# Kernel optimization log

Hardware: AMD Instinct MI355X
Metric: run time of the kernel (lower is better)

Reference implementation:

```python
import jax, jax.numpy as jnp
import numpy as np

B, T, N, D = 256, 200, 8, 64
MODEL = N * D          # 512
FFN_H = 1024 * N // 4  # 2048
EPS = 1.1920929e-07    # torch.finfo(float32).eps (nn.RMSNorm default eps=None)


def setup_inputs() -> dict:
    key = jax.random.key(0)
    ks = jax.random.split(key, 9)
    def xavier(k, shape):
        fan_in, fan_out = shape[-2], shape[-1]
        lim = float(np.sqrt(6.0 / (fan_in + fan_out)))
        return jax.random.uniform(k, shape, jnp.float32, -lim, lim)
    q = jax.random.normal(ks[0], (B, N, D), jnp.float32)
    seq = jax.random.normal(ks[1], (B, T, MODEL), jnp.float32)
    seq_mask = jax.random.randint(ks[2], (B, T), 0, 2) > 0
    seq_mask = seq_mask.at[:, 0].set(True)  # ensure >=1 valid position per row
    return {
        "q": q,
        "seq": seq,
        "rms_w": jnp.ones((MODEL,), jnp.float32),
        "w1": xavier(ks[3], (MODEL, FFN_H)),
        "w2": xavier(ks[4], (MODEL, FFN_H)),
        "w3": xavier(ks[5], (FFN_H, MODEL)),
        "w_k": xavier(ks[6], (N, D, D)),
        "w_v": xavier(ks[7], (N, D, D)),
        "seq_mask": seq_mask,
    }


def reference(q, seq, rms_w, w1, w2, w3, w_k, w_v, seq_mask):
    # RMSNorm
    sn = seq * jax.lax.rsqrt(jnp.mean(seq * seq, axis=-1, keepdims=True) + EPS) * rms_w
    # SwiGLU FFN + residual (dropout=0 / eval)
    h = (jax.nn.silu(sn @ w1) * (sn @ w2)) @ w3 + seq  # (B,T,N*D)
    hh = h.reshape(B, T, N, D)
    keys = jnp.einsum('btnd,nde->bnte', hh, w_k)    # (B,N,T,D)
    values = jnp.einsum('btnd,nde->bnte', hh, w_v)  # (B,N,T,D)
    scale = D ** (-0.5)
    scores = jnp.einsum('bnd,bntd->bnt', q, keys) * scale  # single-query attention
    scores = jnp.where(seq_mask[:, None, :], scores, -jnp.inf)
    attn = jax.nn.softmax(scores, axis=-1)
    ctx = jnp.einsum('bnt,bntd->bnd', attn, values)
    return ctx + q
```

## Files before the change

### kernel.cpp

```cpp
#include <hip/hip_runtime.h>
#include <hip/hip_fp16.h>
#include <cstdint>
#include <cstddef>

typedef unsigned short u16t;
typedef __bf16 bf16x8 __attribute__((ext_vector_type(8)));
typedef float f32x4 __attribute__((ext_vector_type(4)));
typedef unsigned short u16x8 __attribute__((ext_vector_type(8)));

#define BT_ROWS 51200
#define MODEL 512
#define FFNH 2048

__device__ __forceinline__ float bf2f(u16t u) {
  union { unsigned int i; float f; } v; v.i = ((unsigned int)u) << 16; return v.f;
}
__device__ __forceinline__ u16t f2bf(float f) {
  union { float f; unsigned int i; } v; v.f = f;
  return (u16t)((v.i + 0x7fffu + ((v.i >> 16) & 1u)) >> 16);
}
__device__ __forceinline__ float ldf(const void* p, size_t i, int dt) {
  if (dt == 1) return ((const float*)p)[i];
  u16t u = ((const u16t*)p)[i];
  if (dt == 0) return bf2f(u);
  __half h; *(u16t*)&h = u; return __half2float(h);
}
__device__ __forceinline__ void stf(void* p, size_t i, int dt, float f) {
  if (dt == 1) { ((float*)p)[i] = f; }
  else if (dt == 0) { ((u16t*)p)[i] = f2bf(f); }
  else { __half h = __float2half(f); ((u16t*)p)[i] = *(u16t*)&h; }
}
__device__ __forceinline__ void gl2lds16(const void* g, void* l) {
  __builtin_amdgcn_global_load_lds((const __attribute__((address_space(1))) void*)g,
                                   (__attribute__((address_space(3))) void*)l, 16, 0, 0);
}

__device__ __forceinline__ int detect_dt_inline(const unsigned int* __restrict__ w1p) {
  int lane = threadIdx.x & 63;
  unsigned int w = w1p[lane];
  u16t lo = (u16t)(w & 0xffffu), hi = (u16t)(w >> 16);
  float flo = bf2f(lo);
  __half hh; *(u16t*)&hh = hi; float fhi = __half2float(hh);
  int afire = (!(fabsf(flo) < 0.25f)) ? 1 : 0;
  int bfire = (fabsf(fhi) > 0.25f && fabsf(fhi) < 256.f) ? 1 : 0;
  int A = __popcll(__ballot(afire));
  int B = __popcll(__ballot(bfire));
  return (A > 16) ? 1 : ((B < 16) ? 2 : 0);
}

__device__ __forceinline__ void swz_xy(int& bx, int& by, const int NX) {
  int NY = gridDim.y;
  if ((NY & 3) != 0) return;
  int lid = by * NX + bx;
  int k = lid & 7, j = lid >> 3;
  const int hx = NX >> 1;
  bx = (k & 1) * hx + (j % hx);
  by = (k >> 1) * (NY >> 2) + (j / hx);
}

__global__ __launch_bounds__(256) void detect_mask_k(const unsigned int* __restrict__ msk,
                                                     int* __restrict__ flag) {
  __shared__ int sh[4];
  int bad = 0;
  for (int it = 0; it < 50; it++) bad |= (msk[it * 256 + threadIdx.x] > 1u) ? 1 : 0;
  unsigned long long bl = __ballot(bad);
  int w = threadIdx.x >> 6;
  if ((threadIdx.x & 63) == 0) sh[w] = (bl != 0ull) ? 1 : 0;
  __syncthreads();
  if (threadIdx.x == 0) flag[0] = sh[0] | sh[1] | sh[2] | sh[3];
}

__global__ __launch_bounds__(256) void rmsnorm_k(const void* __restrict__ seq,
                                                 const void* __restrict__ w,
                                                 const unsigned int* __restrict__ w1p,
                                                 u16t* __restrict__ xn) {
  const int dt = detect_dt_inline(w1p);
  int row = blockIdx.x * 4 + (threadIdx.x >> 6);
  int lane = threadIdx.x & 63;
  size_t base = (size_t)row * MODEL + lane * 8;
  float x[8]; float ss = 0.f;
  if (dt == 0) {
    u16x8 xv = *(const u16x8*)((const u16t*)seq + base);
#pragma unroll
    for (int j = 0; j < 8; j++) { x[j] = bf2f(xv[j]); ss += x[j] * x[j]; }
  } else if (dt == 1) {
    const f32x4* p = (const f32x4*)((const float*)seq + base);
    f32x4 va = p[0], vb = p[1];
#pragma unroll
    for (int j = 0; j < 4; j++) { x[j] = va[j]; x[4 + j] = vb[j]; }
#pragma unroll
    for (int j = 0; j < 8; j++) ss += x[j] * x[j];
  } else {
#pragma unroll
    for (int j = 0; j < 8; j++) { x[j] = ldf(seq, base + j, dt); ss += x[j] * x[j]; }
  }
#pragma unroll
  for (int o = 32; o; o >>= 1) ss += __shfl_xor(ss, o);
  float rstd = rsqrtf(ss * (1.f / 512.f) + 1.1920929e-07f);
  u16x8 ov;
#pragma unroll
  for (int j = 0; j < 8; j++) ov[j] = f2bf(x[j] * rstd * ldf(w, lane * 8 + j, dt));
  *(u16x8*)(xn + base) = ov;
}

__global__ __launch_bounds__(256) void transpose3_k(const void* __restrict__ w1,
                                                    const void* __restrict__ w2,
                                                    const void* __restrict__ w3,
                                                    u16t* __restrict__ W1t,
                                                    u16t* __restrict__ W2t,
                                                    u16t* __restrict__ W3t) {
  const int dt = detect_dt_inline((const unsigned int*)w1);
  __shared__ u16t tile[32][33];
  int bid = blockIdx.x;
  const void* src; u16t* dst; int R, C, bx, by;
  if (bid < 1024)      { src = w1; dst = W1t; R = MODEL; C = FFNH; bx = bid & 63; by = bid >> 6; }
  else if (bid < 2048) { int t = bid - 1024; src = w2; dst = W2t; R = MODEL; C = FFNH; bx = t & 63; by = t >> 6; }
  else                 { int t = bid - 2048; src = w3; dst = W3t; R = FFNH; C = MODEL; bx = t & 15; by = t >> 4; }
  int x = threadIdx.x & 31, y = threadIdx.x >> 5;
  int c0 = bx * 32, r0 = by * 32;
#pragma unroll
  for (int i = 0; i < 32; i += 8)
    tile[y + i][x] = f2bf(ldf(src, (size_t)(r0 + y + i) * C + c0 + x, dt));
  __syncthreads();
#pragma unroll
  for (int i = 0; i < 32; i += 8) dst[(size_t)(c0 + y + i) * R + r0 + x] = tile[x][y + i];
}


__global__ __launch_bounds__(256, 4) void ffn_gemm1(const u16t* __restrict__ Xn,
                                                    const u16t* __restrict__ W1t,
                                                    const u16t* __restrict__ W2t,
                                                    u16t* __restrict__ Act) {
  __shared__ u16t As[128 * 64];
  __shared__ u16t B1s[64 * 64];
  __shared__ u16t B2s[64 * 64];
  const int tid = threadIdx.x;
  const int lane = tid & 63;
  const int wave = tid >> 6;
  const int wr = wave >> 1, wc = wave & 1;
  const int quad = lane >> 4, l16 = lane & 15;
  int bx = blockIdx.x, by = blockIdx.y;
  swz_xy(bx, by, 32);
  const int nBase = bx * 64;
  const int mBase = by * 128;
  const int wuBase = tid & ~63;

  f32x4 acc1[4][2], acc2[4][2];
  const f32x4 zf = {0.f, 0.f, 0.f, 0.f};
#pragma unroll
  for (int i = 0; i < 4; i++)
#pragma unroll
    for (int j = 0; j < 2; j++) { acc1[i][j] = zf; acc2[i][j] = zf; }

  for (int kt = 0; kt < MODEL; kt += 64) {
#pragma unroll
    for (int c = 0; c < 4; c++) {
      int chunk = c * 256 + tid;
      int r = chunk >> 3, k8 = (chunk & 7) ^ (r & 7);
      gl2lds16(Xn + (size_t)(mBase + r) * MODEL + kt + k8 * 8, As + (size_t)(c * 256 + wuBase) * 8);
    }
#pragma unroll
    for (int c = 0; c < 2; c++) {
      int chunk = c * 256 + tid;
      int r = chunk >> 3, k8 = (chunk & 7) ^ (r & 7);
      gl2lds16(W1t + (size_t)(nBase + r) * MODEL + kt + k8 * 8, B1s + (size_t)(c * 256 + wuBase) * 8);
      gl2lds16(W2t + (size_t)(nBase + r) * MODEL + kt + k8 * 8, B2s + (size_t)(c * 256 + wuBase) * 8);
    }
    __syncthreads();
#pragma unroll
    for (int ks = 0; ks < 64; ks += 32) {
      bf16x8 a[4], b1[2], b2[2];
      const int sw = (ks >> 3) + quad;
#pragma unroll
      for (int mi = 0; mi < 4; mi++) {
        int row = wr * 64 + mi * 16 + l16;
        a[mi] = *(const bf16x8*)(As + row * 64 + ((sw ^ (row & 7)) << 3));
      }
#pragma unroll
      for (int ni = 0; ni < 2; ni++) {
        int row = wc * 32 + ni * 16 + l16;
        b1[ni] = *(const bf16x8*)(B1s + row * 64 + ((sw ^ (row & 7)) << 3));
        b2[ni] = *(const bf16x8*)(B2s + row * 64 + ((sw ^ (row & 7)) << 3));
      }
#pragma unroll
      for (int mi = 0; mi < 4; mi++)
#pragma unroll
        for (int ni = 0; ni < 2; ni++) {
          acc1[mi][ni] = __builtin_amdgcn_mfma_f32_16x16x32_bf16(a[mi], b1[ni], acc1[mi][ni], 0, 0, 0);
          acc2[mi][ni] = __builtin_amdgcn_mfma_f32_16x16x32_bf16(a[mi], b2[ni], acc2[mi][ni], 0, 0, 0);
        }
    }
    __syncthreads();
  }
#pragma unroll
  for (int mi = 0; mi < 4; mi++)
#pragma unroll
    for (int ni = 0; ni < 2; ni++)
#pragma unroll
      for (int r = 0; r < 4; r++) {
        int row = mBase + wr * 64 + mi * 16 + quad * 4 + r;
        int col = nBase + wc * 32 + ni * 16 + l16;
        float g1 = acc1[mi][ni][r], g2 = acc2[mi][ni][r];
        float sl = g1 / (1.f + __expf(-g1));
        Act[(size_t)row * FFNH + col] = f2bf(sl * g2);
      }
}

__global__ __launch_bounds__(256, 4) void ffn_gemm2(const u16t* __restrict__ Act,
                                                    const u16t* __restrict__ W3t,
                                                    const void* __restrict__ Seq,
                                                    const unsigned int* __restrict__ w1p,
                                                    u16t* __restrict__ H, int rowOff) {
  __shared__ u16t As[128 * 64];
  __shared__ u16t Bs[128 * 64];
  const int dt = detect_dt_inline(w1p);
  const int tid = threadIdx.x;
  const int lane = tid & 63;
  const int wave = tid >> 6;
  const int wr = wave >> 1, wc = wave & 1;
  const int quad = lane >> 4, l16 = lane & 15;
  int bx = blockIdx.x, by = blockIdx.y;
  swz_xy(bx, by, 4);
  const int nBase = bx * 128;
  const int mBase = by * 128;
  const int wuBase = tid & ~63;

  f32x4 acc[4][4];
  const f32x4 zf = {0.f, 0.f, 0.f, 0.f};
#pragma unroll
  for (int i = 0; i < 4; i++)
#pragma unroll
    for (int j = 0; j < 4; j++) acc[i][j] = zf;

  for (int kt = 0; kt < FFNH; kt += 64) {
#pragma unroll
    for (int c = 0; c < 4; c++) {
      int chunk = c * 256 + tid;
      int r = chunk >> 3, k8 = (chunk & 7) ^ (r & 7);
      gl2lds16(Act + (size_t)(mBase + r) * FFNH + kt + k8 * 8, As + (size_t)(c * 256 + wuBase) * 8);
      gl2lds16(W3t + (size_t)(nBase + r) * FFNH + kt + k8 * 8, Bs + (size_t)(c * 256 + wuBase) * 8);
    }
    __syncthreads();
#pragma unroll
    for (int ks = 0; ks < 64; ks += 32) {
      bf16x8 a[4], b[4];
      const int sw = (ks >> 3) + quad;
#pragma unroll
      for (int mi = 0; mi < 4; mi++) {
        int row = wr * 64 + mi * 16 + l16;
        a[mi] = *(const bf16x8*)(As + row * 64 + ((sw ^ (row & 7)) << 3));
      }
#pragma unroll
      for (int ni = 0; ni < 4; ni++) {
        int row = wc * 64 + ni * 16 + l16;
        b[ni] = *(const bf16x8*)(Bs + row * 64 + ((sw ^ (row & 7)) << 3));
      }
#pragma unroll
      for (int mi = 0; mi < 4; mi++)
#pragma unroll
        for (int ni = 0; ni < 4; ni++)
          acc[mi][ni] = __builtin_amdgcn_mfma_f32_16x16x32_bf16(a[mi], b[ni], acc[mi][ni], 0, 0, 0);
    }
    __syncthreads();
  }
#pragma unroll
  for (int mi = 0; mi < 4; mi++)
#pragma unroll
    for (int ni = 0; ni < 4; ni++)
#pragma unroll
      for (int r = 0; r < 4; r++) {
        int grow = rowOff + mBase + wr * 64 + mi * 16 + quad * 4 + r;
        int col = nBase + wc * 64 + ni * 16 + l16;
        float v = acc[mi][ni][r] + ldf(Seq, (size_t)grow * MODEL + col, dt);
        H[(size_t)grow * MODEL + col] = f2bf(v);
      }
}

__global__ __launch_bounds__(256) void attn_k(const u16t* __restrict__ H,
                                              const void* __restrict__ q,
                                              const void* __restrict__ wk,
                                              const void* __restrict__ wv,
                                              const int* __restrict__ mask,
                                              const int* __restrict__ mflagp,
                                              const unsigned int* __restrict__ w1p,
                                              void* __restrict__ out) {
  const int b = blockIdx.x >> 3;
  const int n = blockIdx.x & 7;
  const int tid = threadIdx.x;
  const int w = tid >> 6;
  const int lane = tid & 63;
  const int T = 200;
  const int HS = 66;
  const int dt = detect_dt_inline(w1p);
  const int mflag = mflagp[0];

  __shared__ u16t hbuf[200 * HS];
  __shared__ float qk[64];
  __shared__ float sc[200];
  __shared__ float part[256];
  __shared__ float red[8];
  __shared__ float ctx[64];

  for (int chunk = tid; chunk < 1600; chunk += 256) {
    int r = chunk >> 3, c = (chunk & 7) << 3;
    u16x8 v = *(const u16x8*)(H + (size_t)(b * 200 + r) * MODEL + n * 64 + c);
#pragma unroll
    for (int j = 0; j < 8; j++) hbuf[r * HS + c + j] = v[j];
  }

  {
    int d = tid >> 2, sub = tid & 3;
    float s = 0.f;
    size_t wb = ((size_t)n * 64 + d) * 64 + sub * 16;
    size_t qb = (size_t)(b * 8 + n) * 64 + sub * 16;
#pragma unroll
    for (int i = 0; i < 16; i++) s += ldf(wk, wb + i, dt) * ldf(q, qb + i, dt);
    part[tid] = s;
  }
  __syncthreads();
  if (tid < 64) qk[tid] = part[tid * 4] + part[tid * 4 + 1] + part[tid * 4 + 2] + part[tid * 4 + 3];
  __syncthreads();

  float sv = -INFINITY;
  if (tid < T) {
    float s = 0.f;
#pragma unroll 16
    for (int d = 0; d < 64; d++) s += bf2f(hbuf[tid * HS + d]) * qk[d];
    int mv = mflag ? (int)((const unsigned char*)mask)[b * 200 + tid] : mask[b * 200 + tid];
    sv = mv ? s * 0.125f : -INFINITY;
  }

  float mx = sv;
#pragma unroll
  for (int o = 32; o; o >>= 1) mx = fmaxf(mx, __shfl_xor(mx, o));
  if (lane == 0) red[w] = mx;
  __syncthreads();
  float gmax = fmaxf(fmaxf(red[0], red[1]), fmaxf(red[2], red[3]));
  float e = 0.f;
  if (gmax == -INFINITY) {
    if (tid == 0) e = 1.f;
  } else if (tid < T) {
    e = __expf(sv - gmax);
  }
  float s = e;
#pragma unroll
  for (int o = 32; o; o >>= 1) s += __shfl_xor(s, o);
  if (lane == 0) red[4 + w] = s;
  __syncthreads();
  float inv = 1.f / (red[4] + red[5] + red[6] + red[7]);
  if (tid < T) sc[tid] = e * inv;
  __syncthreads();

  float a2 = 0.f;
  for (int t = w; t < T; t += 4) a2 += sc[t] * bf2f(hbuf[t * HS + lane]);
  part[tid] = a2;
  __syncthreads();
  if (tid < 64) ctx[tid] = part[tid] + part[64 + tid] + part[128 + tid] + part[192 + tid];
  __syncthreads();

  {
    int od = tid & 63;
    float s2 = 0.f;
#pragma unroll
    for (int i = 0; i < 16; i++) {
      int d = w * 16 + i;
      s2 += ctx[d] * ldf(wv, ((size_t)n * 64 + d) * 64 + od, dt);
    }
    part[tid] = s2;
  }
  __syncthreads();
  if (tid < 64) {
    size_t oi = (size_t)(b * 8 + n) * 64 + tid;
    stf(out, oi, dt,
        part[tid] + part[64 + tid] + part[128 + tid] + part[192 + tid] + ldf(q, oi, dt));
  }
}

extern "C" void kernel_launch(void* const* d_in, const int* in_sizes, int n_in,
                              void* d_out, int out_size, void* d_ws, size_t ws_size,
                              hipStream_t stream) {
  (void)in_sizes; (void)n_in; (void)out_size;
  const void* q   = d_in[0];
  const void* seq = d_in[1];
  const void* rw  = d_in[2];
  const void* w1  = d_in[3];
  const void* w2  = d_in[4];
  const void* w3  = d_in[5];
  const void* wk  = d_in[6];
  const void* wv  = d_in[7];
  const int*  msk = (const int*)d_in[8];

  char* ws = (char*)d_ws;
  size_t off = 0;
  auto alloc = [&](size_t b) { void* p = ws + off; off = (off + b + 255) & ~(size_t)255; return p; };
  int*  flags = (int*)alloc(512);
  int*  mflag = flags + 0;
  u16t* Xn  = (u16t*)alloc((size_t)BT_ROWS * MODEL * 2);
  u16t* W1t = (u16t*)alloc((size_t)FFNH * MODEL * 2);
  u16t* W2t = (u16t*)alloc((size_t)FFNH * MODEL * 2);
  u16t* W3t = (u16t*)alloc((size_t)MODEL * FFNH * 2);
  size_t actBytes = (ws_size > off) ? (ws_size - off) : 0;
  long tpc = (long)(actBytes / ((size_t)128 * FFNH * 2));
  if (tpc < 1) tpc = 1;
  if (tpc > 200) tpc = 200;
  u16t* ActB = (u16t*)(ws + off);

  detect_mask_k<<<dim3(1), dim3(256), 0, stream>>>((const unsigned int*)msk, mflag);
  rmsnorm_k<<<dim3(BT_ROWS / 4), dim3(256), 0, stream>>>(seq, rw, (const unsigned int*)w1, Xn);
  transpose3_k<<<dim3(3072), dim3(256), 0, stream>>>(w1, w2, w3, W1t, W2t, W3t);

  for (int t0 = 0; t0 < 400; t0 += (int)tpc) {
    int tiles = (400 - t0 < (int)tpc) ? (400 - t0) : (int)tpc;
    int rows0 = t0 * 128;
    ffn_gemm1<<<dim3(FFNH / 64, tiles), dim3(256), 0, stream>>>(
        Xn + (size_t)rows0 * MODEL, W1t, W2t, ActB);
    ffn_gemm2<<<dim3(MODEL / 128, tiles), dim3(256), 0, stream>>>(
        ActB, W3t, seq, (const unsigned int*)w1, Xn, rows0);
  }
  attn_k<<<dim3(2048), dim3(256), 0, stream>>>(Xn, q, wk, wv, msk, mflag,
                                               (const unsigned int*)w1, d_out);
}
```

Before: 634.4 us.

## Merge front-end kernels into one launch and remap block ids for XCD locality

Folds the mask detection, RMSNorm and weight-transpose kernels into a single front_k launch, with block-id ranges selecting the role. This removes two kernel launches and the gaps between them. It also replaces the ffn_gemm2 swizzle and remaps attention block ids so blocks that share inputs land on the same XCD under round-robin dispatch. The merged kernel uses a shared-memory tile in only some of its branches, and the remapped ids assume grid sizes divisible by 8.

```diff
diff --git a/kernel.cpp b/kernel.cpp
--- a/kernel.cpp
+++ b/kernel.cpp
@@ -58,72 +58,73 @@
   by = (k >> 1) * (NY >> 2) + (j / hx);
 }
 
-__global__ __launch_bounds__(256) void detect_mask_k(const unsigned int* __restrict__ msk,
-                                                     int* __restrict__ flag) {
-  __shared__ int sh[4];
-  int bad = 0;
-  for (int it = 0; it < 50; it++) bad |= (msk[it * 256 + threadIdx.x] > 1u) ? 1 : 0;
-  unsigned long long bl = __ballot(bad);
-  int w = threadIdx.x >> 6;
-  if ((threadIdx.x & 63) == 0) sh[w] = (bl != 0ull) ? 1 : 0;
-  __syncthreads();
-  if (threadIdx.x == 0) flag[0] = sh[0] | sh[1] | sh[2] | sh[3];
-}
-
-__global__ __launch_bounds__(256) void rmsnorm_k(const void* __restrict__ seq,
-                                                 const void* __restrict__ w,
-                                                 const unsigned int* __restrict__ w1p,
-                                                 u16t* __restrict__ xn) {
-  const int dt = detect_dt_inline(w1p);
-  int row = blockIdx.x * 4 + (threadIdx.x >> 6);
-  int lane = threadIdx.x & 63;
-  size_t base = (size_t)row * MODEL + lane * 8;
-  float x[8]; float ss = 0.f;
-  if (dt == 0) {
-    u16x8 xv = *(const u16x8*)((const u16t*)seq + base);
-#pragma unroll
-    for (int j = 0; j < 8; j++) { x[j] = bf2f(xv[j]); ss += x[j] * x[j]; }
-  } else if (dt == 1) {
-    const f32x4* p = (const f32x4*)((const float*)seq + base);
-    f32x4 va = p[0], vb = p[1];
-#pragma unroll
-    for (int j = 0; j < 4; j++) { x[j] = va[j]; x[4 + j] = vb[j]; }
-#pragma unroll
-    for (int j = 0; j < 8; j++) ss += x[j] * x[j];
+__global__ __launch_bounds__(256) void front_k(const void* __restrict__ seq,
+                                               const void* __restrict__ rw,
+                                               const void* __restrict__ w1,
+                                               const void* __restrict__ w2,
+                                               const void* __restrict__ w3,
+                                               u16t* __restrict__ W1t,
+                                               u16t* __restrict__ W2t,
+                                               u16t* __restrict__ W3t,
+                                               const unsigned int* __restrict__ msk,
+                                               int* __restrict__ mflag,
+                                               u16t* __restrict__ xn) {
+  const unsigned int* w1p = (const unsigned int*)w1;
+  int bid = blockIdx.x;
+  if (bid < 12800) {
+    const int dt = detect_dt_inline(w1p);
+    int row = bid * 4 + (threadIdx.x >> 6);
+    int lane = threadIdx.x & 63;
+    size_t base = (size_t)row * MODEL + lane * 8;
+    float x[8]; float ss = 0.f;
+    if (dt == 0) {
+      u16x8 xv = *(const u16x8*)((const u16t*)seq + base);
+#pragma unroll
+      for (int j = 0; j < 8; j++) { x[j] = bf2f(xv[j]); ss += x[j] * x[j]; }
+    } else if (dt == 1) {
+      const f32x4* p = (const f32x4*)((const float*)seq + base);
+      f32x4 va = p[0], vb = p[1];
+#pragma unroll
+      for (int j = 0; j < 4; j++) { x[j] = va[j]; x[4 + j] = vb[j]; }
+#pragma unroll
+      for (int j = 0; j < 8; j++) ss += x[j] * x[j];
+    } else {
+#pragma unroll
+      for (int j = 0; j < 8; j++) { x[j] = ldf(seq, base + j, dt); ss += x[j] * x[j]; }
+    }
+#pragma unroll
+    for (int o = 32; o; o >>= 1) ss += __shfl_xor(ss, o);
+    float rstd = rsqrtf(ss * (1.f / 512.f) + 1.1920929e-07f);
+    u16x8 ov;
+#pragma unroll
+    for (int j = 0; j < 8; j++) ov[j] = f2bf(x[j] * rstd * ldf(rw, lane * 8 + j, dt));
+    *(u16x8*)(xn + base) = ov;
+  } else if (bid < 12800 + 3072) {
+    const int dt = detect_dt_inline(w1p);
+    __shared__ u16t tile[32][33];
+    int t = bid - 12800;
+    const void* src; u16t* dst; int R, C, bx, by;
+    if (t < 1024)      { src = w1; dst = W1t; R = MODEL; C = FFNH; bx = t & 63; by = t >> 6; }
+    else if (t < 2048) { t -= 1024; src = w2; dst = W2t; R = MODEL; C = FFNH; bx = t & 63; by = t >> 6; }
+    else               { t -= 2048; src = w3; dst = W3t; R = FFNH; C = MODEL; bx = t & 15; by = t >> 4; }
+    int x = threadIdx.x & 31, y = threadIdx.x >> 5;
+    int c0 = bx * 32, r0 = by * 32;
+#pragma unroll
+    for (int i = 0; i < 32; i += 8)
+      tile[y + i][x] = f2bf(ldf(src, (size_t)(r0 + y + i) * C + c0 + x, dt));
+    __syncthreads();
+#pragma unroll
+    for (int i = 0; i < 32; i += 8) dst[(size_t)(c0 + y + i) * R + r0 + x] = tile[x][y + i];
   } else {
-#pragma unroll
-    for (int j = 0; j < 8; j++) { x[j] = ldf(seq, base + j, dt); ss += x[j] * x[j]; }
-  }
-#pragma unroll
-  for (int o = 32; o; o >>= 1) ss += __shfl_xor(ss, o);
-  float rstd = rsqrtf(ss * (1.f / 512.f) + 1.1920929e-07f);
-  u16x8 ov;
-#pragma unroll
-  for (int j = 0; j < 8; j++) ov[j] = f2bf(x[j] * rstd * ldf(w, lane * 8 + j, dt));
-  *(u16x8*)(xn + base) = ov;
-}
-
-__global__ __launch_bounds__(256) void transpose3_k(const void* __restrict__ w1,
-                                                    const void* __restrict__ w2,
-                                                    const void* __restrict__ w3,
-                                                    u16t* __restrict__ W1t,
-                                                    u16t* __restrict__ W2t,
-                                                    u16t* __restrict__ W3t) {
-  const int dt = detect_dt_inline((const unsigned int*)w1);
-  __shared__ u16t tile[32][33];
-  int bid = blockIdx.x;
-  const void* src; u16t* dst; int R, C, bx, by;
-  if (bid < 1024)      { src = w1; dst = W1t; R = MODEL; C = FFNH; bx = bid & 63; by = bid >> 6; }
-  else if (bid < 2048) { int t = bid - 1024; src = w2; dst = W2t; R = MODEL; C = FFNH; bx = t & 63; by = t >> 6; }
-  else                 { int t = bid - 2048; src = w3; dst = W3t; R = FFNH; C = MODEL; bx = t & 15; by = t >> 4; }
-  int x = threadIdx.x & 31, y = threadIdx.x >> 5;
-  int c0 = bx * 32, r0 = by * 32;
-#pragma unroll
-  for (int i = 0; i < 32; i += 8)
-    tile[y + i][x] = f2bf(ldf(src, (size_t)(r0 + y + i) * C + c0 + x, dt));
-  __syncthreads();
-#pragma unroll
-  for (int i = 0; i < 32; i += 8) dst[(size_t)(c0 + y + i) * R + r0 + x] = tile[x][y + i];
+    __shared__ int sh[4];
+    int bad = 0;
+    for (int it = 0; it < 50; it++) bad |= (msk[it * 256 + threadIdx.x] > 1u) ? 1 : 0;
+    unsigned long long bl = __ballot(bad);
+    int w = threadIdx.x >> 6;
+    if ((threadIdx.x & 63) == 0) sh[w] = (bl != 0ull) ? 1 : 0;
+    __syncthreads();
+    if (threadIdx.x == 0) mflag[0] = sh[0] | sh[1] | sh[2] | sh[3];
+  }
 }
 
 
@@ -220,7 +221,12 @@
   const int wr = wave >> 1, wc = wave & 1;
   const int quad = lane >> 4, l16 = lane & 15;
   int bx = blockIdx.x, by = blockIdx.y;
-  swz_xy(bx, by, 4);
+  if ((gridDim.y & 7) == 0) {
+    int lid = by * 4 + bx;
+    int k = lid & 7, j = lid >> 3;
+    bx = j & 3;
+    by = (j >> 2) * 8 + k;
+  }
   const int nBase = bx * 128;
   const int mBase = by * 128;
   const int wuBase = tid & ~63;
@@ -284,8 +290,10 @@
                                               const int* __restrict__ mflagp,
                                               const unsigned int* __restrict__ w1p,
                                               void* __restrict__ out) {
-  const int b = blockIdx.x >> 3;
-  const int n = blockIdx.x & 7;
+  int lid = blockIdx.x;
+  int xk = lid & 7, xj = lid >> 3;
+  const int n = xj & 7;
+  const int b = (xj >> 3) * 8 + xk;
   const int tid = threadIdx.x;
   const int w = tid >> 6;
   const int lane = tid & 63;
@@ -405,9 +413,8 @@
   if (tpc > 200) tpc = 200;
   u16t* ActB = (u16t*)(ws + off);
 
-  detect_mask_k<<<dim3(1), dim3(256), 0, stream>>>((const unsigned int*)msk, mflag);
-  rmsnorm_k<<<dim3(BT_ROWS / 4), dim3(256), 0, stream>>>(seq, rw, (const unsigned int*)w1, Xn);
-  transpose3_k<<<dim3(3072), dim3(256), 0, stream>>>(w1, w2, w3, W1t, W2t, W3t);
+  front_k<<<dim3(12800 + 3072 + 1), dim3(256), 0, stream>>>(
+      seq, rw, w1, w2, w3, W1t, W2t, W3t, (const unsigned int*)msk, mflag, Xn);
 
   for (int t0 = 0; t0 < 400; t0 += (int)tpc) {
     int tiles = (400 - t0 < (int)tpc) ? (400 - t0) : (int)tpc;
```

Result: no change. 639.4 us (+0.8%).
